# Optimization experiments

Hardware: AMD Instinct MI355X
Metric: run time of the kernel (lower is better)

Reference implementation:

```python
import jax, jax.numpy as jnp
import numpy as np

N_HOPS = 6
NEG_INF = -1e30


def setup_inputs() -> dict:
    key = jax.random.key(0)
    ks = jax.random.split(key, 12)
    B, L, T, V, D, C = 64, 512, 8, 50000, 1024, 3
    context_ids = jax.random.randint(ks[0], (B, L), 0, V, dtype=jnp.int32)
    target_ids = jax.random.randint(ks[1], (B, T), 0, V, dtype=jnp.int32)
    context_len = jax.random.randint(ks[2], (B,), 256, L + 1, dtype=jnp.int32)
    target_len = jax.random.randint(ks[3], (B,), 2, T + 1, dtype=jnp.int32)
    target_offset = jax.random.randint(ks[4], (B,), 0, 256, dtype=jnp.int32)
    s = 0.02
    return {
        "context_ids": context_ids,
        "target_ids": target_ids,
        "context_len": context_len,
        "target_len": target_len,
        "target_offset": target_offset,
        "embedding_matrix": jax.random.normal(ks[5], (V, D), jnp.float32) * s,
        "W_lin": jax.random.normal(ks[6], (D, D), jnp.float32) * s,
        "b_lin": jax.random.normal(ks[7], (D,), jnp.float32) * s,
        "w_attn": jax.random.normal(ks[8], (2 * D, 1), jnp.float32) * s,
        "b_attn": jax.random.normal(ks[9], (1,), jnp.float32) * s,
        "W_out": jax.random.normal(ks[10], (D, C), jnp.float32) * s,
        "b_out": jax.random.normal(ks[11], (C,), jnp.float32) * s,
    }


def reference(context_ids, target_ids, context_len, target_len, target_offset,
              embedding_matrix, W_lin, b_lin, w_attn, b_attn, W_out, b_out):
    B, L = context_ids.shape
    T = target_ids.shape[1]

    pos = jnp.arange(L, dtype=jnp.int32)[None, :]            # [1,L]
    ctx_mask = pos < context_len[:, None]                    # [B,L] valid positions

    # location model 2: v_i = 1 - |i - target_offset| / seq_len, zeroed off-sequence
    dist = jnp.abs(pos - target_offset[:, None]).astype(jnp.float32)
    v_loc = (1.0 - dist / context_len[:, None].astype(jnp.float32))
    v_loc = jnp.where(ctx_mask, v_loc, 0.0)                  # [B,L]

    memory = embedding_matrix[context_ids]                   # [B,L,D]
    ext_memory = memory * v_loc[..., None]                   # [B,L,D] (loc-model-2 branch)

    # v_aspect: variable-length mean of target embeddings
    tgt_emb = embedding_matrix[target_ids]                   # [B,T,D]
    t_mask = (jnp.arange(T, dtype=jnp.int32)[None, :] < target_len[:, None])
    v_aspect = (tgt_emb * t_mask[..., None].astype(jnp.float32)).sum(axis=1)
    v_aspect = v_aspect / target_len[:, None].astype(jnp.float32)  # [B,D]

    vec = v_aspect
    for _ in range(N_HOPS):  # fixed hop count; linear + attn params shared (AUTO_REUSE)
        lin = vec @ W_lin + b_lin                            # [B,D]
        # content attention: tanh(W [m_i ; v] + b) scores
        s_mem = jnp.einsum('bld,dk->bl', ext_memory, w_attn[: ext_memory.shape[-1]])
        s_vec = vec @ w_attn[ext_memory.shape[-1]:]          # [B,1]
        scores = jnp.tanh(s_mem + s_vec + b_attn[0])         # [B,L]
        scores = jnp.where(ctx_mask, scores, NEG_INF)
        alpha = jax.nn.softmax(scores, axis=-1)              # [B,L]
        attn_out = jnp.einsum('bl,bld->bd', alpha, ext_memory)
        vec = attn_out + lin

    logits = vec @ W_out + b_out                             # [B,C]
    return logits
```

## Files before the change

kernel.cpp:

```cpp
#include <hip/hip_runtime.h>
#include <cstdint>


#define DD 1024
#define LL 512
#define BB 64
#define MTS 32

__global__ __launch_bounds__(256) void k_init(const float* __restrict__ w_attn,
                                              const float* __restrict__ W_out,
                                              float* __restrict__ Mt,
                                              float* __restrict__ Mc)
{
  int d = blockIdx.x * 256 + threadIdx.x;
  float w0 = w_attn[d];
  float u0 = w_attn[DD + d];
  Mt[d * MTS + 0] = w0; Mc[0 * DD + d] = w0;
  Mt[d * MTS + 1] = u0; Mc[1 * DD + d] = u0;
#pragma unroll
  for (int c = 0; c < 3; ++c) {
    float y = W_out[d * 3 + c];
    int col = 7 + 6 * c;
    Mt[d * MTS + col] = y; Mc[col * DD + d] = y;
  }
}

__global__ __launch_bounds__(256) void k_chain(const float* __restrict__ Wl,
                                               float* __restrict__ Mt,
                                               float* __restrict__ Mc,
                                               int i0, int i1, int i2, int i3,
                                               int o0, int o1, int o2, int o3)
{
  int tid = threadIdx.x;
  int wv = __builtin_amdgcn_readfirstlane(tid >> 6);
  int ln = tid & 63;
  int i = blockIdx.x * 4 + wv;
  const float* wrow = Wl + (size_t)i * DD;
  int c0 = i0 < 0 ? 0 : i0, c1 = i1 < 0 ? 0 : i1;
  int c2 = i2 < 0 ? 0 : i2, c3 = i3 < 0 ? 0 : i3;
  float s0 = 0.f, s1 = 0.f, s2 = 0.f, s3 = 0.f;
  for (int m = 0; m < 16; ++m) {
    int j = ln + m * 64;
    float w = wrow[j];
    s0 += w * Mc[c0 * DD + j];
    s1 += w * Mc[c1 * DD + j];
    s2 += w * Mc[c2 * DD + j];
    s3 += w * Mc[c3 * DD + j];
  }
#pragma unroll
  for (int m = 1; m < 64; m <<= 1) {
    s0 += __shfl_xor(s0, m, 64); s1 += __shfl_xor(s1, m, 64);
    s2 += __shfl_xor(s2, m, 64); s3 += __shfl_xor(s3, m, 64);
  }
  if (ln == 0) {
    if (o0 >= 0) { Mt[i * MTS + o0] = s0; Mc[o0 * DD + i] = s0; }
    if (o1 >= 0) { Mt[i * MTS + o1] = s1; Mc[o1 * DD + i] = s1; }
    if (o2 >= 0) { Mt[i * MTS + o2] = s2; Mc[o2 * DD + i] = s2; }
    if (o3 >= 0) { Mt[i * MTS + o3] = s3; Mc[o3 * DD + i] = s3; }
  }
}

__global__ __launch_bounds__(256, 2) void k_gemm(const int* __restrict__ ctx_ids,
                                                 const int* __restrict__ ctx_len,
                                                 const int* __restrict__ toff,
                                                 const float* __restrict__ emb,
                                                 const float* __restrict__ Mt,
                                                 float* __restrict__ Q)
{
  __shared__ float stag[4][64 * 33];
  __shared__ float qp[4][64][25];
  int tid = threadIdx.x;
  int kq = __builtin_amdgcn_readfirstlane(tid >> 6);
  int ln = tid & 63;
  int rowbase = blockIdx.x * 64;
  int myid = ctx_ids[rowbase + ln];
  const float* base[8];
#pragma unroll
  for (int ii = 0; ii < 8; ++ii) {
    int rid = __shfl(myid, ii * 8 + (ln >> 3), 64);
    base[ii] = emb + (size_t)rid * DD;
  }
  int p4 = (ln & 7) * 4;
  float* sw = stag[kq];
  int k0 = kq * 256;
  float acc[25];
#pragma unroll
  for (int j = 0; j < 25; ++j) acc[j] = 0.f;

  float4 buf[8];
#pragma unroll
  for (int ii = 0; ii < 8; ++ii)
    buf[ii] = *(const float4*)(base[ii] + k0 + p4);

  for (int ch = 0; ch < 8; ++ch) {
#pragma unroll
    for (int ii = 0; ii < 8; ++ii) {
      int r = ii * 8 + (ln >> 3);
      int a = r * 33 + p4;
      sw[a + 0] = buf[ii].x; sw[a + 1] = buf[ii].y;
      sw[a + 2] = buf[ii].z; sw[a + 3] = buf[ii].w;
    }
    if (ch < 7) {
      int kb = k0 + (ch + 1) * 32;
#pragma unroll
      for (int ii = 0; ii < 8; ++ii)
        buf[ii] = *(const float4*)(base[ii] + kb + p4);
    }
    __builtin_amdgcn_s_waitcnt(0xc07f);
    const float* mrow = Mt + (size_t)(k0 + ch * 32) * MTS;
#pragma unroll 4
    for (int kk = 0; kk < 32; ++kk) {
      float mv = sw[ln * 33 + kk];
#pragma unroll
      for (int j = 0; j < 25; ++j) acc[j] += mv * mrow[kk * MTS + j];
    }
  }
#pragma unroll
  for (int j = 0; j < 25; ++j) qp[kq][ln][j] = acc[j];
  __syncthreads();

  int b = rowbase >> 9;
  int l0 = rowbase & 511;
  int clen = ctx_len[b];
  int off = toff[b];
  float fclen = (float)clen;
  for (int i = tid; i < 1600; i += 256) {
    int j = i >> 6, r = i & 63;
    float s = qp[0][r][j] + qp[1][r][j] + qp[2][r][j] + qp[3][r][j];
    int l = l0 + r;
    float vl = (l < clen) ? (1.f - fabsf((float)(l - off)) / fclen) : 0.f;
    Q[((size_t)b * 25 + j) * LL + l] = s * vl;
  }
}

template <bool ISMAX>
__device__ __forceinline__ void breduce(float* v, int n, float* lds, int tid)
{
  int wv = __builtin_amdgcn_readfirstlane(tid >> 6);
  int ln = tid & 63;
  for (int q = 0; q < n; ++q) {
    float x = v[q];
#pragma unroll
    for (int m = 1; m < 64; m <<= 1) {
      float o = __shfl_xor(x, m, 64);
      x = ISMAX ? fmaxf(x, o) : x + o;
    }
    if (ln == 0) lds[q * 4 + wv] = x;
  }
  __syncthreads();
  for (int q = 0; q < n; ++q) {
    float a = lds[q * 4 + 0], b = lds[q * 4 + 1];
    float c = lds[q * 4 + 2], d = lds[q * 4 + 3];
    v[q] = ISMAX ? fmaxf(fmaxf(a, b), fmaxf(c, d)) : ((a + b) + (c + d));
  }
  __syncthreads();
}

__global__ __launch_bounds__(256) void k_hop(const int* __restrict__ tgt_ids,
                                             const int* __restrict__ tgt_len,
                                             const int* __restrict__ ctx_len,
                                             const float* __restrict__ emb,
                                             const float* __restrict__ b_lin,
                                             const float* __restrict__ b_attn,
                                             const float* __restrict__ b_out,
                                             const float* __restrict__ Mc,
                                             const float* __restrict__ Q,
                                             float* __restrict__ out)
{
  __shared__ float Qs[25 * LL];
  __shared__ float va[DD];
  __shared__ float red[36 * 4];
  int tid = threadIdx.x;
  int b = blockIdx.x;

  for (int i = tid; i < 25 * LL; i += 256) Qs[i] = Q[(size_t)b * (25 * LL) + i];

  int tl = tgt_len[b];
  float inv_tl = 1.f / (float)tl;
  for (int d = tid; d < DD; d += 256) {
    float s = 0.f;
#pragma unroll
    for (int t = 0; t < 8; ++t)
      if (t < tl) s += emb[(size_t)tgt_ids[b * 8 + t] * DD + d];
    va[d] = s * inv_tl;
  }
  __syncthreads();

  float p[32];
#pragma unroll
  for (int q = 0; q < 32; ++q) p[q] = 0.f;
  for (int d = tid; d < DD; d += 256) {
    float vad = va[d], bd = b_lin[d];
#pragma unroll
    for (int k = 0; k < 6; ++k) {
      float u = Mc[(1 + k) * DD + d];
      p[k] += vad * u;
      if (k < 5) p[9 + k] += bd * u;
    }
#pragma unroll
    for (int c = 0; c < 3; ++c) {
      p[6 + c] += vad * Mc[(25 + c) * DD + d];
#pragma unroll
      for (int k = 0; k < 6; ++k)
        p[14 + c * 6 + k] += bd * Mc[(7 + 6 * c + k) * DD + d];
    }
  }
  breduce<false>(p, 32, red, tid);

  float tcur[6], rc[3], beta[5], gam[18];
#pragma unroll
  for (int k = 0; k < 6; ++k) tcur[k] = p[k];
#pragma unroll
  for (int c = 0; c < 3; ++c) rc[c] = p[6 + c];
#pragma unroll
  for (int k = 0; k < 5; ++k) beta[k] = p[9 + k];
#pragma unroll
  for (int q = 0; q < 18; ++q) gam[q] = p[14 + q];

  int clen = ctx_len[b];
  float batt = b_attn[0];
  int l1 = tid, l2 = tid + 256;

  for (int h = 0; h < 6; ++h) {
    float s_h = tcur[0];
    float sc1 = -1e30f, sc2 = -1e30f;
    if (l1 < clen) sc1 = tanhf(Qs[l1] + s_h + batt);
    if (l2 < clen) sc2 = tanhf(Qs[l2] + s_h + batt);
    float mx = fmaxf(sc1, sc2);
    breduce<true>(&mx, 1, red, tid);

    float pe[9];
#pragma unroll
    for (int q = 0; q < 9; ++q) pe[q] = 0.f;
    int kd = 5 - h;
    if (l1 < clen) {
      float e = expf(sc1 - mx);
      pe[0] += e;
      for (int k = 0; k <= 4 - h; ++k) pe[1 + k] += e * Qs[(1 + k) * LL + l1];
#pragma unroll
      for (int c = 0; c < 3; ++c) pe[6 + c] += e * Qs[(7 + 6 * c + kd) * LL + l1];
    }
    if (l2 < clen) {
      float e = expf(sc2 - mx);
      pe[0] += e;
      for (int k = 0; k <= 4 - h; ++k) pe[1 + k] += e * Qs[(1 + k) * LL + l2];
#pragma unroll
      for (int c = 0; c < 3; ++c) pe[6 + c] += e * Qs[(7 + 6 * c + kd) * LL + l2];
    }
    breduce<false>(pe, 9, red, tid);

    float invS = 1.f / pe[0];
    for (int k = 0; k <= 4 - h; ++k)
      tcur[k] = pe[1 + k] * invS + tcur[k + 1] + beta[k];
#pragma unroll
    for (int c = 0; c < 3; ++c)
      rc[c] = pe[6 + c] * invS + rc[c] + gam[c * 6 + kd];
  }
  if (tid < 3) out[b * 3 + tid] = rc[tid] + b_out[tid];
}

extern "C" void kernel_launch(void* const* d_in, const int* in_sizes, int n_in,
                              void* d_out, int out_size, void* d_ws, size_t ws_size,
                              hipStream_t stream)
{
  const int*   ctx_ids = (const int*)d_in[0];
  const int*   tgt_ids = (const int*)d_in[1];
  const int*   ctx_len = (const int*)d_in[2];
  const int*   tgt_len = (const int*)d_in[3];
  const int*   toff    = (const int*)d_in[4];
  const float* emb     = (const float*)d_in[5];
  const float* Wl      = (const float*)d_in[6];
  const float* bl      = (const float*)d_in[7];
  const float* wat     = (const float*)d_in[8];
  const float* bat     = (const float*)d_in[9];
  const float* Wo      = (const float*)d_in[10];
  const float* bo      = (const float*)d_in[11];
  float* ws = (float*)d_ws;
  float* Mt = ws;
  float* Mc = ws + 32768;
  float* Q  = ws + 65536;
  float* outp = (float*)d_out;

  hipLaunchKernelGGL(k_init, dim3(4), dim3(256), 0, stream, wat, Wo, Mt, Mc);
  for (int s = 1; s <= 6; ++s) {
    int i0 = (s <= 5) ? s : -1;
    int o0 = (s <= 5) ? (1 + s) : -1;
    int i1 = 6 + s,  o1 = (s <= 5) ? (7 + s)  : 25;
    int i2 = 12 + s, o2 = (s <= 5) ? (13 + s) : 26;
    int i3 = 18 + s, o3 = (s <= 5) ? (19 + s) : 27;
    hipLaunchKernelGGL(k_chain, dim3(256), dim3(256), 0, stream,
                       Wl, Mt, Mc, i0, i1, i2, i3, o0, o1, o2, o3);
  }
  hipLaunchKernelGGL(k_gemm, dim3(512), dim3(256), 0, stream,
                     ctx_ids, ctx_len, toff, emb, Mt, Q);
  hipLaunchKernelGGL(k_hop, dim3(64), dim3(256), 0, stream,
                     tgt_ids, tgt_len, ctx_len, emb, bl, bat, bo, Mc, Q, outp);
}
```

Before: 366.8 us.

## Fuse all stages into one persistent kernel with grid barriers and embedding prefetch

Replaces the nine separate launches (init, six W_lin chain steps, the gather-GEMM and the hop kernel) with one 512-block persistent kernel. The stages are separated by atomic-counter grid barriers, and the shared memory of the GEMM and hop phases is overlaid in a union. While the small chain phases run, each block touches slices of its context embedding rows so they are warm in cache for the GEMM. This removes per-launch overhead and idle gaps between dependent stages. In exchange it relies on all 512 blocks being co-resident, adds spin-wait barrier costs, and the chain work now runs on only half the waves of each block.

Measured after the change: 767.2 us. 109% more time.

```diff
diff --git a/kernel.cpp b/kernel.cpp
--- a/kernel.cpp
+++ b/kernel.cpp
@@ -4,133 +4,53 @@
 
 #define DD 1024
 #define LL 512
-#define BB 64
 #define MTS 32
-
-__global__ __launch_bounds__(256) void k_init(const float* __restrict__ w_attn,
-                                              const float* __restrict__ W_out,
-                                              float* __restrict__ Mt,
-                                              float* __restrict__ Mc)
-{
-  int d = blockIdx.x * 256 + threadIdx.x;
-  float w0 = w_attn[d];
-  float u0 = w_attn[DD + d];
-  Mt[d * MTS + 0] = w0; Mc[0 * DD + d] = w0;
-  Mt[d * MTS + 1] = u0; Mc[1 * DD + d] = u0;
-#pragma unroll
-  for (int c = 0; c < 3; ++c) {
-    float y = W_out[d * 3 + c];
-    int col = 7 + 6 * c;
-    Mt[d * MTS + col] = y; Mc[col * DD + d] = y;
-  }
-}
-
-__global__ __launch_bounds__(256) void k_chain(const float* __restrict__ Wl,
-                                               float* __restrict__ Mt,
-                                               float* __restrict__ Mc,
-                                               int i0, int i1, int i2, int i3,
-                                               int o0, int o1, int o2, int o3)
-{
-  int tid = threadIdx.x;
-  int wv = __builtin_amdgcn_readfirstlane(tid >> 6);
-  int ln = tid & 63;
-  int i = blockIdx.x * 4 + wv;
-  const float* wrow = Wl + (size_t)i * DD;
-  int c0 = i0 < 0 ? 0 : i0, c1 = i1 < 0 ? 0 : i1;
-  int c2 = i2 < 0 ? 0 : i2, c3 = i3 < 0 ? 0 : i3;
-  float s0 = 0.f, s1 = 0.f, s2 = 0.f, s3 = 0.f;
-  for (int m = 0; m < 16; ++m) {
-    int j = ln + m * 64;
-    float w = wrow[j];
-    s0 += w * Mc[c0 * DD + j];
-    s1 += w * Mc[c1 * DD + j];
-    s2 += w * Mc[c2 * DD + j];
-    s3 += w * Mc[c3 * DD + j];
-  }
-#pragma unroll
-  for (int m = 1; m < 64; m <<= 1) {
-    s0 += __shfl_xor(s0, m, 64); s1 += __shfl_xor(s1, m, 64);
-    s2 += __shfl_xor(s2, m, 64); s3 += __shfl_xor(s3, m, 64);
-  }
-  if (ln == 0) {
-    if (o0 >= 0) { Mt[i * MTS + o0] = s0; Mc[o0 * DD + i] = s0; }
-    if (o1 >= 0) { Mt[i * MTS + o1] = s1; Mc[o1 * DD + i] = s1; }
-    if (o2 >= 0) { Mt[i * MTS + o2] = s2; Mc[o2 * DD + i] = s2; }
-    if (o3 >= 0) { Mt[i * MTS + o3] = s3; Mc[o3 * DD + i] = s3; }
-  }
-}
-
-__global__ __launch_bounds__(256, 2) void k_gemm(const int* __restrict__ ctx_ids,
-                                                 const int* __restrict__ ctx_len,
-                                                 const int* __restrict__ toff,
-                                                 const float* __restrict__ emb,
-                                                 const float* __restrict__ Mt,
-                                                 float* __restrict__ Q)
-{
-  __shared__ float stag[4][64 * 33];
-  __shared__ float qp[4][64][25];
-  int tid = threadIdx.x;
-  int kq = __builtin_amdgcn_readfirstlane(tid >> 6);
-  int ln = tid & 63;
-  int rowbase = blockIdx.x * 64;
-  int myid = ctx_ids[rowbase + ln];
-  const float* base[8];
-#pragma unroll
-  for (int ii = 0; ii < 8; ++ii) {
-    int rid = __shfl(myid, ii * 8 + (ln >> 3), 64);
-    base[ii] = emb + (size_t)rid * DD;
-  }
-  int p4 = (ln & 7) * 4;
-  float* sw = stag[kq];
-  int k0 = kq * 256;
-  float acc[25];
-#pragma unroll
-  for (int j = 0; j < 25; ++j) acc[j] = 0.f;
-
-  float4 buf[8];
-#pragma unroll
-  for (int ii = 0; ii < 8; ++ii)
-    buf[ii] = *(const float4*)(base[ii] + k0 + p4);
-
-  for (int ch = 0; ch < 8; ++ch) {
-#pragma unroll
-    for (int ii = 0; ii < 8; ++ii) {
-      int r = ii * 8 + (ln >> 3);
-      int a = r * 33 + p4;
-      sw[a + 0] = buf[ii].x; sw[a + 1] = buf[ii].y;
-      sw[a + 2] = buf[ii].z; sw[a + 3] = buf[ii].w;
-    }
-    if (ch < 7) {
-      int kb = k0 + (ch + 1) * 32;
-#pragma unroll
-      for (int ii = 0; ii < 8; ++ii)
-        buf[ii] = *(const float4*)(base[ii] + kb + p4);
-    }
-    __builtin_amdgcn_s_waitcnt(0xc07f);
-    const float* mrow = Mt + (size_t)(k0 + ch * 32) * MTS;
-#pragma unroll 4
-    for (int kk = 0; kk < 32; ++kk) {
-      float mv = sw[ln * 33 + kk];
-#pragma unroll
-      for (int j = 0; j < 25; ++j) acc[j] += mv * mrow[kk * MTS + j];
-    }
-  }
-#pragma unroll
-  for (int j = 0; j < 25; ++j) qp[kq][ln][j] = acc[j];
+#define NBLK 512u
+
+__device__ unsigned g_cnt[8];
+
+__device__ __forceinline__ void gbar(int k)
+{
   __syncthreads();
-
-  int b = rowbase >> 9;
-  int l0 = rowbase & 511;
-  int clen = ctx_len[b];
-  int off = toff[b];
-  float fclen = (float)clen;
-  for (int i = tid; i < 1600; i += 256) {
-    int j = i >> 6, r = i & 63;
-    float s = qp[0][r][j] + qp[1][r][j] + qp[2][r][j] + qp[3][r][j];
-    int l = l0 + r;
-    float vl = (l < clen) ? (1.f - fabsf((float)(l - off)) / fclen) : 0.f;
-    Q[((size_t)b * 25 + j) * LL + l] = s * vl;
-  }
+  if (threadIdx.x == 0) {
+    __threadfence();
+    unsigned t = __hip_atomic_fetch_add(&g_cnt[k], 1u, __ATOMIC_RELAXED,
+                                        __HIP_MEMORY_SCOPE_AGENT);
+    unsigned tgt = (t / NBLK + 1u) * NBLK;
+    int guard = 0;
+    while (__hip_atomic_load(&g_cnt[k], __ATOMIC_RELAXED,
+                             __HIP_MEMORY_SCOPE_AGENT) < tgt) {
+      __builtin_amdgcn_s_sleep(2);
+      if (++guard > (1 << 22)) break;
+    }
+    __threadfence();
+  }
+  __syncthreads();
+}
+
+union SMem {
+  struct { float stag[4][64 * 33]; float qp[4][64][25]; } g;
+  struct { float Qs[25 * LL]; float va[DD]; float red[36 * 4]; } h;
+};
+
+__device__ __forceinline__ void keep4(float4 v) {
+  asm volatile("" :: "v"(v.x), "v"(v.y), "v"(v.z), "v"(v.w));
+}
+
+__device__ __forceinline__ void prefetch10(const int* __restrict__ ctx_ids,
+                                           const float* __restrict__ emb,
+                                           int rowbase, int tid, int ph)
+{
+  float4 v[10];
+  int r0 = ph * 10;
+#pragma unroll
+  for (int rr = 0; rr < 10; ++rr) {
+    int r = r0 + rr; if (r > 63) r = 63;
+    int rid = ctx_ids[rowbase + r];
+    v[rr] = ((const float4*)(emb + (size_t)rid * DD))[tid];
+  }
+#pragma unroll
+  for (int rr = 0; rr < 10; ++rr) keep4(v[rr]);
 }
 
 template <bool ISMAX>
@@ -156,107 +76,228 @@
   __syncthreads();
 }
 
-__global__ __launch_bounds__(256) void k_hop(const int* __restrict__ tgt_ids,
-                                             const int* __restrict__ tgt_len,
-                                             const int* __restrict__ ctx_len,
-                                             const float* __restrict__ emb,
-                                             const float* __restrict__ b_lin,
-                                             const float* __restrict__ b_attn,
-                                             const float* __restrict__ b_out,
-                                             const float* __restrict__ Mc,
-                                             const float* __restrict__ Q,
-                                             float* __restrict__ out)
-{
-  __shared__ float Qs[25 * LL];
-  __shared__ float va[DD];
-  __shared__ float red[36 * 4];
-  int tid = threadIdx.x;
-  int b = blockIdx.x;
-
-  for (int i = tid; i < 25 * LL; i += 256) Qs[i] = Q[(size_t)b * (25 * LL) + i];
-
-  int tl = tgt_len[b];
-  float inv_tl = 1.f / (float)tl;
-  for (int d = tid; d < DD; d += 256) {
-    float s = 0.f;
-#pragma unroll
-    for (int t = 0; t < 8; ++t)
-      if (t < tl) s += emb[(size_t)tgt_ids[b * 8 + t] * DD + d];
-    va[d] = s * inv_tl;
-  }
-  __syncthreads();
-
-  float p[32];
-#pragma unroll
-  for (int q = 0; q < 32; ++q) p[q] = 0.f;
-  for (int d = tid; d < DD; d += 256) {
-    float vad = va[d], bd = b_lin[d];
-#pragma unroll
-    for (int k = 0; k < 6; ++k) {
-      float u = Mc[(1 + k) * DD + d];
-      p[k] += vad * u;
-      if (k < 5) p[9 + k] += bd * u;
-    }
+__global__ __launch_bounds__(256, 2) void k_all(
+    const int* __restrict__ ctx_ids, const int* __restrict__ tgt_ids,
+    const int* __restrict__ ctx_len, const int* __restrict__ tgt_len,
+    const int* __restrict__ toff,    const float* __restrict__ emb,
+    const float* __restrict__ Wl,    const float* __restrict__ bl,
+    const float* __restrict__ wat,   const float* __restrict__ bat,
+    const float* __restrict__ bo,    const float* __restrict__ Wo,
+    float* __restrict__ Mt, float* __restrict__ Mc,
+    float* __restrict__ Q,  float* __restrict__ out)
+{
+  __shared__ SMem sm;
+  const int tid = threadIdx.x;
+  const int bid = blockIdx.x;
+  const int wv  = __builtin_amdgcn_readfirstlane(tid >> 6);
+  const int ln  = tid & 63;
+  const int rowbase = bid * 64;
+
+  if (bid < 4) {
+    int d = bid * 256 + tid;
+    float w0 = wat[d], u0 = wat[DD + d];
+    Mt[d * MTS + 0] = w0; Mc[0 * DD + d] = w0;
+    Mt[d * MTS + 1] = u0; Mc[1 * DD + d] = u0;
 #pragma unroll
     for (int c = 0; c < 3; ++c) {
-      p[6 + c] += vad * Mc[(25 + c) * DD + d];
-#pragma unroll
-      for (int k = 0; k < 6; ++k)
-        p[14 + c * 6 + k] += bd * Mc[(7 + 6 * c + k) * DD + d];
-    }
-  }
-  breduce<false>(p, 32, red, tid);
-
-  float tcur[6], rc[3], beta[5], gam[18];
-#pragma unroll
-  for (int k = 0; k < 6; ++k) tcur[k] = p[k];
-#pragma unroll
-  for (int c = 0; c < 3; ++c) rc[c] = p[6 + c];
-#pragma unroll
-  for (int k = 0; k < 5; ++k) beta[k] = p[9 + k];
-#pragma unroll
-  for (int q = 0; q < 18; ++q) gam[q] = p[14 + q];
-
-  int clen = ctx_len[b];
-  float batt = b_attn[0];
-  int l1 = tid, l2 = tid + 256;
-
-  for (int h = 0; h < 6; ++h) {
-    float s_h = tcur[0];
-    float sc1 = -1e30f, sc2 = -1e30f;
-    if (l1 < clen) sc1 = tanhf(Qs[l1] + s_h + batt);
-    if (l2 < clen) sc2 = tanhf(Qs[l2] + s_h + batt);
-    float mx = fmaxf(sc1, sc2);
-    breduce<true>(&mx, 1, red, tid);
-
-    float pe[9];
-#pragma unroll
-    for (int q = 0; q < 9; ++q) pe[q] = 0.f;
-    int kd = 5 - h;
-    if (l1 < clen) {
-      float e = expf(sc1 - mx);
-      pe[0] += e;
-      for (int k = 0; k <= 4 - h; ++k) pe[1 + k] += e * Qs[(1 + k) * LL + l1];
-#pragma unroll
-      for (int c = 0; c < 3; ++c) pe[6 + c] += e * Qs[(7 + 6 * c + kd) * LL + l1];
-    }
-    if (l2 < clen) {
-      float e = expf(sc2 - mx);
-      pe[0] += e;
-      for (int k = 0; k <= 4 - h; ++k) pe[1 + k] += e * Qs[(1 + k) * LL + l2];
-#pragma unroll
-      for (int c = 0; c < 3; ++c) pe[6 + c] += e * Qs[(7 + 6 * c + kd) * LL + l2];
-    }
-    breduce<false>(pe, 9, red, tid);
-
-    float invS = 1.f / pe[0];
-    for (int k = 0; k <= 4 - h; ++k)
-      tcur[k] = pe[1 + k] * invS + tcur[k + 1] + beta[k];
-#pragma unroll
-    for (int c = 0; c < 3; ++c)
-      rc[c] = pe[6 + c] * invS + rc[c] + gam[c * 6 + kd];
-  }
-  if (tid < 3) out[b * 3 + tid] = rc[tid] + b_out[tid];
+      float y = Wo[d * 3 + c];
+      int col = 7 + 6 * c;
+      Mt[d * MTS + col] = y; Mc[col * DD + d] = y;
+    }
+  }
+  prefetch10(ctx_ids, emb, rowbase, tid, 0);
+  gbar(0);
+
+  for (int s = 1; s <= 6; ++s) {
+    if (wv < 2) {
+      int i = bid * 2 + wv;
+      const float* wrow = Wl + (size_t)i * DD;
+      int c0 = (s <= 5) ? s : 0;
+      int c1 = 6 + s, c2 = 12 + s, c3 = 18 + s;
+      float s0 = 0.f, s1 = 0.f, s2 = 0.f, s3 = 0.f;
+      for (int m = 0; m < 16; ++m) {
+        int j = ln + m * 64;
+        float w = wrow[j];
+        s0 += w * Mc[c0 * DD + j];
+        s1 += w * Mc[c1 * DD + j];
+        s2 += w * Mc[c2 * DD + j];
+        s3 += w * Mc[c3 * DD + j];
+      }
+#pragma unroll
+      for (int m = 1; m < 64; m <<= 1) {
+        s0 += __shfl_xor(s0, m, 64); s1 += __shfl_xor(s1, m, 64);
+        s2 += __shfl_xor(s2, m, 64); s3 += __shfl_xor(s3, m, 64);
+      }
+      if (ln == 0) {
+        if (s <= 5) { Mt[i * MTS + 1 + s] = s0; Mc[(1 + s) * DD + i] = s0; }
+        int o1 = (s <= 5) ? 7 + s  : 25;
+        int o2 = (s <= 5) ? 13 + s : 26;
+        int o3 = (s <= 5) ? 19 + s : 27;
+        Mt[i * MTS + o1] = s1; Mc[o1 * DD + i] = s1;
+        Mt[i * MTS + o2] = s2; Mc[o2 * DD + i] = s2;
+        Mt[i * MTS + o3] = s3; Mc[o3 * DD + i] = s3;
+      }
+    }
+    prefetch10(ctx_ids, emb, rowbase, tid, s);
+    gbar(s);
+  }
+
+  {
+    float* sw = sm.g.stag[wv];
+    int myid = ctx_ids[rowbase + ln];
+    const float* base[8];
+#pragma unroll
+    for (int ii = 0; ii < 8; ++ii) {
+      int rid = __shfl(myid, ii * 8 + (ln >> 3), 64);
+      base[ii] = emb + (size_t)rid * DD;
+    }
+    int p4 = (ln & 7) * 4;
+    int k0 = wv * 256;
+    float acc[25];
+#pragma unroll
+    for (int j = 0; j < 25; ++j) acc[j] = 0.f;
+
+    float4 buf[8];
+#pragma unroll
+    for (int ii = 0; ii < 8; ++ii)
+      buf[ii] = *(const float4*)(base[ii] + k0 + p4);
+
+    for (int ch = 0; ch < 8; ++ch) {
+#pragma unroll
+      for (int ii = 0; ii < 8; ++ii) {
+        int r = ii * 8 + (ln >> 3);
+        int a = r * 33 + p4;
+        sw[a + 0] = buf[ii].x; sw[a + 1] = buf[ii].y;
+        sw[a + 2] = buf[ii].z; sw[a + 3] = buf[ii].w;
+      }
+      if (ch < 7) {
+        int kb = k0 + (ch + 1) * 32;
+#pragma unroll
+        for (int ii = 0; ii < 8; ++ii)
+          buf[ii] = *(const float4*)(base[ii] + kb + p4);
+      }
+      __builtin_amdgcn_s_waitcnt(0xc07f);
+      const float* mrow = Mt + (size_t)(k0 + ch * 32) * MTS;
+#pragma unroll 4
+      for (int kk = 0; kk < 32; ++kk) {
+        float mv = sw[ln * 33 + kk];
+#pragma unroll
+        for (int j = 0; j < 25; ++j) acc[j] += mv * mrow[kk * MTS + j];
+      }
+    }
+#pragma unroll
+    for (int j = 0; j < 25; ++j) sm.g.qp[wv][ln][j] = acc[j];
+    __syncthreads();
+
+    int b = rowbase >> 9;
+    int l0 = rowbase & 511;
+    int clen = ctx_len[b];
+    int off = toff[b];
+    float fclen = (float)clen;
+    for (int i = tid; i < 1600; i += 256) {
+      int j = i >> 6, r = i & 63;
+      float s = sm.g.qp[0][r][j] + sm.g.qp[1][r][j] +
+                sm.g.qp[2][r][j] + sm.g.qp[3][r][j];
+      int l = l0 + r;
+      float vl = (l < clen) ? (1.f - fabsf((float)(l - off)) / fclen) : 0.f;
+      Q[((size_t)b * 25 + j) * LL + l] = s * vl;
+    }
+  }
+  gbar(7);
+
+  if (bid >= 64) return;
+  {
+    float* Qs = sm.h.Qs;
+    float* va = sm.h.va;
+    float* red = sm.h.red;
+    int b = bid;
+
+    for (int i = tid; i < 25 * LL; i += 256)
+      Qs[i] = Q[(size_t)b * (25 * LL) + i];
+
+    int tl = tgt_len[b];
+    float inv_tl = 1.f / (float)tl;
+    for (int d = tid; d < DD; d += 256) {
+      float s = 0.f;
+#pragma unroll
+      for (int t = 0; t < 8; ++t)
+        if (t < tl) s += emb[(size_t)tgt_ids[b * 8 + t] * DD + d];
+      va[d] = s * inv_tl;
+    }
+    __syncthreads();
+
+    float p[32];
+#pragma unroll
+    for (int q = 0; q < 32; ++q) p[q] = 0.f;
+    for (int d = tid; d < DD; d += 256) {
+      float vad = va[d], bd = bl[d];
+#pragma unroll
+      for (int k = 0; k < 6; ++k) {
+        float u = Mc[(1 + k) * DD + d];
+        p[k] += vad * u;
+        if (k < 5) p[9 + k] += bd * u;
+      }
+#pragma unroll
+      for (int c = 0; c < 3; ++c) {
+        p[6 + c] += vad * Mc[(25 + c) * DD + d];
+#pragma unroll
+        for (int k = 0; k < 6; ++k)
+          p[14 + c * 6 + k] += bd * Mc[(7 + 6 * c + k) * DD + d];
+      }
+    }
+    breduce<false>(p, 32, red, tid);
+
+    float tcur[6], rc[3], beta[5], gam[18];
+#pragma unroll
+    for (int k = 0; k < 6; ++k) tcur[k] = p[k];
+#pragma unroll
+    for (int c = 0; c < 3; ++c) rc[c] = p[6 + c];
+#pragma unroll
+    for (int k = 0; k < 5; ++k) beta[k] = p[9 + k];
+#pragma unroll
+    for (int q = 0; q < 18; ++q) gam[q] = p[14 + q];
+
+    int clen = ctx_len[b];
+    float batt = bat[0];
+    int l1 = tid, l2 = tid + 256;
+
+    for (int h = 0; h < 6; ++h) {
+      float s_h = tcur[0];
+      float sc1 = -1e30f, sc2 = -1e30f;
+      if (l1 < clen) sc1 = tanhf(Qs[l1] + s_h + batt);
+      if (l2 < clen) sc2 = tanhf(Qs[l2] + s_h + batt);
+      float mx = fmaxf(sc1, sc2);
+      breduce<true>(&mx, 1, red, tid);
+
+      float pe[9];
+#pragma unroll
+      for (int q = 0; q < 9; ++q) pe[q] = 0.f;
+      int kd = 5 - h;
+      if (l1 < clen) {
+        float e = expf(sc1 - mx);
+        pe[0] += e;
+        for (int k = 0; k <= 4 - h; ++k) pe[1 + k] += e * Qs[(1 + k) * LL + l1];
+#pragma unroll
+        for (int c = 0; c < 3; ++c) pe[6 + c] += e * Qs[(7 + 6 * c + kd) * LL + l1];
+      }
+      if (l2 < clen) {
+        float e = expf(sc2 - mx);
+        pe[0] += e;
+        for (int k = 0; k <= 4 - h; ++k) pe[1 + k] += e * Qs[(1 + k) * LL + l2];
+#pragma unroll
+        for (int c = 0; c < 3; ++c) pe[6 + c] += e * Qs[(7 + 6 * c + kd) * LL + l2];
+      }
+      breduce<false>(pe, 9, red, tid);
+
+      float invS = 1.f / pe[0];
+      for (int k = 0; k <= 4 - h; ++k)
+        tcur[k] = pe[1 + k] * invS + tcur[k + 1] + beta[k];
+#pragma unroll
+      for (int c = 0; c < 3; ++c)
+        rc[c] = pe[6 + c] * invS + rc[c] + gam[c * 6 + kd];
+    }
+    if (tid < 3) out[b * 3 + tid] = rc[tid] + bo[tid];
+  }
 }
 
 extern "C" void kernel_launch(void* const* d_in, const int* in_sizes, int n_in,
@@ -281,18 +322,7 @@
   float* Q  = ws + 65536;
   float* outp = (float*)d_out;
 
-  hipLaunchKernelGGL(k_init, dim3(4), dim3(256), 0, stream, wat, Wo, Mt, Mc);
-  for (int s = 1; s <= 6; ++s) {
-    int i0 = (s <= 5) ? s : -1;
-    int o0 = (s <= 5) ? (1 + s) : -1;
-    int i1 = 6 + s,  o1 = (s <= 5) ? (7 + s)  : 25;
-    int i2 = 12 + s, o2 = (s <= 5) ? (13 + s) : 26;
-    int i3 = 18 + s, o3 = (s <= 5) ? (19 + s) : 27;
-    hipLaunchKernelGGL(k_chain, dim3(256), dim3(256), 0, stream,
-                       Wl, Mt, Mc, i0, i1, i2, i3, o0, o1, o2, o3);
-  }
-  hipLaunchKernelGGL(k_gemm, dim3(512), dim3(256), 0, stream,
-                     ctx_ids, ctx_len, toff, emb, Mt, Q);
-  hipLaunchKernelGGL(k_hop, dim3(64), dim3(256), 0, stream,
-                     tgt_ids, tgt_len, ctx_len, emb, bl, bat, bo, Mc, Q, outp);
-}
+  hipLaunchKernelGGL(k_all, dim3(512), dim3(256), 0, stream,
+                     ctx_ids, tgt_ids, ctx_len, tgt_len, toff, emb,
+                     Wl, bl, wat, bat, bo, Wo, Mt, Mc, Q, outp);
+}
```
